# Optimization experiments

Measured on AMD Instinct MI355X. Metric: run time of the kernel, lower is better.

## Reference

```python
import jax, jax.numpy as jnp
import numpy as np

S, C, HD = 2048, 3072, 128
H = C // HD  # 24 heads
EPS = 1e-6


def setup_inputs() -> dict:
    key = jax.random.key(0)
    ks = jax.random.split(key, 12)
    x = jax.random.normal(ks[0], (S, C), dtype=jnp.float32)
    rope = jax.random.normal(ks[1], (S, 1, HD // 2, 2, 2), dtype=jnp.float32)
    w = 0.02
    return {
        "x": x,
        "rope": rope,
        "wq": jax.random.normal(ks[2], (C, C), dtype=jnp.float32) * w,
        "bq": jnp.zeros((C,), dtype=jnp.float32),
        "wk": jax.random.normal(ks[3], (C, C), dtype=jnp.float32) * w,
        "bk": jnp.zeros((C,), dtype=jnp.float32),
        "wv": jax.random.normal(ks[4], (C, C), dtype=jnp.float32) * w,
        "bv": jnp.zeros((C,), dtype=jnp.float32),
        "wo": jax.random.normal(ks[5], (C, C), dtype=jnp.float32) * w,
        "bo": jnp.zeros((C,), dtype=jnp.float32),
        "qn_w": jnp.ones((HD,), dtype=jnp.float32),
        "kn_w": jnp.ones((HD,), dtype=jnp.float32),
    }


def _rmsnorm(t, w):
    # t: [S, H, HD]; normalize over last dim
    ms = jnp.mean(t * t, axis=-1, keepdims=True)
    return t * jax.lax.rsqrt(ms + EPS) * w


def _apply_rotary(t, rope):
    # t: [S, H, HD] -> [S, H, HD//2, 1, 2]; rope: [S, 1, HD//2, 2, 2]
    t_ = t.reshape(S, H, HD // 2, 1, 2)
    out = jnp.sum(rope * t_, axis=-1)  # [S, H, HD//2, 2]
    return out.reshape(S, H, HD)


def reference(x, rope, wq, bq, wk, bk, wv, bv, wo, bo, qn_w, kn_w):
    q = (x @ wq.T + bq).reshape(S, H, HD)
    k = (x @ wk.T + bk).reshape(S, H, HD)
    v = (x @ wv.T + bv).reshape(S, H, HD)
    q = _rmsnorm(q, qn_w)
    k = _rmsnorm(k, kn_w)
    q = _apply_rotary(q, rope)
    k = _apply_rotary(k, rope)
    # dense SDPA: scores [H, S, S]
    scores = jnp.einsum('shd,thd->hst', q, k) / jnp.sqrt(jnp.float32(HD))
    attn = jax.nn.softmax(scores, axis=-1)
    out = jnp.einsum('hst,thd->shd', attn, v).reshape(S, C)
    return out @ wo.T + bo
```

## Files before the change

kernel.cpp:

```cpp
#include <hip/hip_runtime.h>
#include <cstdint>
#include <cstddef>

#define SS 2048
#define CC 3072
#define HDIM 128
#define NH 24

using bf16 = __bf16;
typedef __bf16 bf16x8 __attribute__((ext_vector_type(8)));
typedef float f32x4 __attribute__((ext_vector_type(4)));

typedef const __attribute__((address_space(1))) void* gas1_cvp;
typedef __attribute__((address_space(3))) void* las3_vp;

__device__ __forceinline__ void gll16(const void* g, void* l) {
  __builtin_amdgcn_global_load_lds((gas1_cvp)g, (las3_vp)l, 16, 0, 0);
}

__device__ __forceinline__ bf16x8 cvt8(f32x4 a, f32x4 b) {
  bf16x8 r;
  r[0] = (bf16)a[0]; r[1] = (bf16)a[1]; r[2] = (bf16)a[2]; r[3] = (bf16)a[3];
  r[4] = (bf16)b[0]; r[5] = (bf16)b[1]; r[6] = (bf16)b[2]; r[7] = (bf16)b[3];
  return r;
}

#define NX ((size_t)SS * CC)
#define NW ((size_t)CC * CC)

__global__ __launch_bounds__(256)
void k_cvt(const float* __restrict__ s0, const float* __restrict__ s1,
           const float* __restrict__ s2, const float* __restrict__ s3,
           const float* __restrict__ s4, bf16* __restrict__ dst) {
  const int z = blockIdx.y;
  const float* src = (z == 0) ? s0 : (z == 1) ? s1 : (z == 2) ? s2 : (z == 3) ? s3 : s4;
  const size_t nz = (z == 0) ? NX : NW;
  const size_t base = (z == 0) ? 0 : NX + (size_t)(z - 1) * NW;
  const size_t i = ((size_t)blockIdx.x * 256 + threadIdx.x) * 8;
  if (i < nz) {
    const f32x4 a = *(const f32x4*)(src + i);
    const f32x4 b = *(const f32x4*)(src + i + 4);
    *(bf16x8*)(dst + base + i) = cvt8(a, b);
  }
}

__device__ __forceinline__ void gemm_bt_bf16(const bf16* __restrict__ A,
                                             const bf16* __restrict__ W,
                                             const float* __restrict__ bias,
                                             void* __restrict__ out,
                                             int M, int N, int K, int mode) {
  __shared__ __align__(16) bf16 As[128][32];
  __shared__ __align__(16) bf16 Ws[128][32];
  const int t = threadIdx.x, wave = t >> 6, lane = t & 63;
  const int m0 = blockIdx.y * 128, n0 = blockIdx.x * 128;
  const int wm = (wave >> 1) * 64, wn = (wave & 1) * 64;
  const int fr = lane & 15, fq = (lane >> 4) * 8;

  f32x4 acc[4][4] = {};

  for (int k0 = 0; k0 < K; k0 += 32) {
    __syncthreads();
#pragma unroll
    for (int it = 0; it < 2; ++it) {
      const int pc = wave * 2 + it;
      const int pi = pc * 64 + lane;
      const int row = pi >> 2, c8 = (pi & 3) * 8;
      gll16(A + (size_t)(m0 + row) * K + (k0 + c8), (char*)&As[0][0] + pc * 1024);
      gll16(W + (size_t)(n0 + row) * K + (k0 + c8), (char*)&Ws[0][0] + pc * 1024);
    }
    __syncthreads();
    bf16x8 a[4], b[4];
#pragma unroll
    for (int i = 0; i < 4; ++i) a[i] = *(const bf16x8*)&As[wm + i * 16 + fr][fq];
#pragma unroll
    for (int j = 0; j < 4; ++j) b[j] = *(const bf16x8*)&Ws[wn + j * 16 + fr][fq];
#pragma unroll
    for (int i = 0; i < 4; ++i)
#pragma unroll
      for (int j = 0; j < 4; ++j)
        acc[i][j] = __builtin_amdgcn_mfma_f32_16x16x32_bf16(a[i], b[j], acc[i][j], 0, 0, 0);
  }

  const int lr4 = (lane >> 4) * 4;
#pragma unroll
  for (int i = 0; i < 4; ++i) {
#pragma unroll
    for (int j = 0; j < 4; ++j) {
      const int col = n0 + wn + j * 16 + fr;
      const float bb = bias[col];
#pragma unroll
      for (int r = 0; r < 4; ++r) {
        const int row = m0 + wm + i * 16 + lr4 + r;
        const float v = acc[i][j][r] + bb;
        if (mode == 0)
          ((bf16*)out)[((size_t)(col >> 7) * M + row) * 128 + (col & 127)] = (bf16)v;
        else if (mode == 1)
          ((bf16*)out)[(size_t)col * M + row] = (bf16)v;
        else
          ((float*)out)[(size_t)row * N + col] = v;
      }
    }
  }
}

__global__ __launch_bounds__(256, 2)
void k_gemm_qkv_b(const bf16* __restrict__ xb,
                  const bf16* __restrict__ wqb, const bf16* __restrict__ wkb,
                  const bf16* __restrict__ wvb,
                  const float* __restrict__ bq, const float* __restrict__ bk,
                  const float* __restrict__ bv,
                  bf16* __restrict__ Qo, bf16* __restrict__ Ko, bf16* __restrict__ Vo) {
  const int z = blockIdx.z;
  const bf16* W  = (z == 0) ? wqb : (z == 1) ? wkb : wvb;
  const float* B = (z == 0) ? bq : (z == 1) ? bk : bv;
  void* O        = (z == 0) ? (void*)Qo : (z == 1) ? (void*)Ko : (void*)Vo;
  gemm_bt_bf16(xb, W, B, O, SS, CC, CC, (z == 2) ? 1 : 0);
}

__global__ __launch_bounds__(256, 2)
void k_gemm_out_b(const bf16* __restrict__ A, const bf16* __restrict__ wob,
                  const float* __restrict__ bo, float* __restrict__ out) {
  gemm_bt_bf16(A, wob, bo, out, SS, CC, CC, 2);
}

template<int AF32>
__device__ __forceinline__ void gemm_core(const void* __restrict__ Ap,
                                          const float* __restrict__ W,
                                          const float* __restrict__ bias,
                                          void* __restrict__ out,
                                          int M, int N, int K, int mode) {
  __shared__ __align__(16) bf16 As[128][32];
  __shared__ __align__(16) bf16 Ws[128][32];
  const int t = threadIdx.x, wave = t >> 6, lane = t & 63;
  const int m0 = blockIdx.y * 128, n0 = blockIdx.x * 128;
  const int wm = (wave >> 1) * 64, wn = (wave & 1) * 64;
  const int fr = lane & 15, fq = (lane >> 4) * 8;
  const int pi0 = wave * 128 + lane;
  const int pi1 = pi0 + 64;
  const int row0 = pi0 >> 2, c0 = (pi0 & 3) * 8;
  const int row1 = pi1 >> 2, c1 = (pi1 & 3) * 8;

  f32x4 raf0[2], raf1[2], rw0[2], rw1[2];
  bf16x8 rab0, rab1;

  auto issue = [&](int k0) {
    if (AF32) {
      const float* A = (const float*)Ap;
      const float* p0 = A + (size_t)(m0 + row0) * K + k0 + c0;
      raf0[0] = *(const f32x4*)p0; raf0[1] = *(const f32x4*)(p0 + 4);
      const float* p1 = A + (size_t)(m0 + row1) * K + k0 + c1;
      raf1[0] = *(const f32x4*)p1; raf1[1] = *(const f32x4*)(p1 + 4);
    } else {
      const bf16* A = (const bf16*)Ap;
      rab0 = *(const bf16x8*)(A + (size_t)(m0 + row0) * K + k0 + c0);
      rab1 = *(const bf16x8*)(A + (size_t)(m0 + row1) * K + k0 + c1);
    }
    const float* q0 = W + (size_t)(n0 + row0) * K + k0 + c0;
    rw0[0] = *(const f32x4*)q0; rw0[1] = *(const f32x4*)(q0 + 4);
    const float* q1 = W + (size_t)(n0 + row1) * K + k0 + c1;
    rw1[0] = *(const f32x4*)q1; rw1[1] = *(const f32x4*)(q1 + 4);
  };

  f32x4 acc[4][4] = {};
  issue(0);
  for (int k0 = 0; k0 < K; k0 += 32) {
    __syncthreads();
    if (AF32) {
      *(bf16x8*)&As[row0][c0] = cvt8(raf0[0], raf0[1]);
      *(bf16x8*)&As[row1][c1] = cvt8(raf1[0], raf1[1]);
    } else {
      *(bf16x8*)&As[row0][c0] = rab0;
      *(bf16x8*)&As[row1][c1] = rab1;
    }
    *(bf16x8*)&Ws[row0][c0] = cvt8(rw0[0], rw0[1]);
    *(bf16x8*)&Ws[row1][c1] = cvt8(rw1[0], rw1[1]);
    __syncthreads();
    if (k0 + 32 < K) issue(k0 + 32);
    bf16x8 a[4], b[4];
#pragma unroll
    for (int i = 0; i < 4; ++i) a[i] = *(const bf16x8*)&As[wm + i * 16 + fr][fq];
#pragma unroll
    for (int j = 0; j < 4; ++j) b[j] = *(const bf16x8*)&Ws[wn + j * 16 + fr][fq];
#pragma unroll
    for (int i = 0; i < 4; ++i)
#pragma unroll
      for (int j = 0; j < 4; ++j)
        acc[i][j] = __builtin_amdgcn_mfma_f32_16x16x32_bf16(a[i], b[j], acc[i][j], 0, 0, 0);
  }

  const int lr4 = (lane >> 4) * 4;
#pragma unroll
  for (int i = 0; i < 4; ++i) {
#pragma unroll
    for (int j = 0; j < 4; ++j) {
      const int col = n0 + wn + j * 16 + fr;
      const float bb = bias[col];
#pragma unroll
      for (int r = 0; r < 4; ++r) {
        const int row = m0 + wm + i * 16 + lr4 + r;
        const float v = acc[i][j][r] + bb;
        if (mode == 0)
          ((bf16*)out)[((size_t)(col >> 7) * M + row) * 128 + (col & 127)] = (bf16)v;
        else if (mode == 1)
          ((bf16*)out)[(size_t)col * M + row] = (bf16)v;
        else
          ((float*)out)[(size_t)row * N + col] = v;
      }
    }
  }
}

__global__ __launch_bounds__(256, 2)
void k_gemm_qkv_f(const float* __restrict__ x,
                  const float* __restrict__ wq, const float* __restrict__ wk,
                  const float* __restrict__ wv,
                  const float* __restrict__ bq, const float* __restrict__ bk,
                  const float* __restrict__ bv,
                  bf16* __restrict__ Qo, bf16* __restrict__ Ko, bf16* __restrict__ Vo) {
  const int z = blockIdx.z;
  const float* W = (z == 0) ? wq : (z == 1) ? wk : wv;
  const float* B = (z == 0) ? bq : (z == 1) ? bk : bv;
  void* O        = (z == 0) ? (void*)Qo : (z == 1) ? (void*)Ko : (void*)Vo;
  gemm_core<1>(x, W, B, O, SS, CC, CC, (z == 2) ? 1 : 0);
}

__global__ __launch_bounds__(256, 2)
void k_gemm_out_f(const bf16* __restrict__ A, const float* __restrict__ wo,
                  const float* __restrict__ bo, float* __restrict__ out) {
  gemm_core<0>(A, wo, bo, out, SS, CC, CC, 2);
}

__global__ __launch_bounds__(256)
void k_norm_rope(bf16* __restrict__ Q, bf16* __restrict__ K,
                 const float* __restrict__ rope,
                 const float* __restrict__ qw, const float* __restrict__ kw) {
  const int t = threadIdx.x, wave = t >> 6, lane = t & 63;
  const int idx = blockIdx.x * 4 + wave;
  const int s = idx / NH, h = idx % NH;
  const size_t base = ((size_t)h * SS + s) * HDIM + 2 * lane;

  bf16 q2[2], k2[2];
  *(uint32_t*)q2 = *(const uint32_t*)(Q + base);
  *(uint32_t*)k2 = *(const uint32_t*)(K + base);
  const float q0 = (float)q2[0], q1 = (float)q2[1];
  const float k0 = (float)k2[0], k1 = (float)k2[1];
  float sq = q0 * q0 + q1 * q1;
  float sk = k0 * k0 + k1 * k1;
#pragma unroll
  for (int m = 1; m < 64; m <<= 1) {
    sq += __shfl_xor(sq, m);
    sk += __shfl_xor(sk, m);
  }
  const float rq = rsqrtf(sq * (1.0f / 128.0f) + 1e-6f);
  const float rk = rsqrtf(sk * (1.0f / 128.0f) + 1e-6f);

  const float qn0 = q0 * rq * qw[2 * lane], qn1 = q1 * rq * qw[2 * lane + 1];
  const float kn0 = k0 * rk * kw[2 * lane], kn1 = k1 * rk * kw[2 * lane + 1];

  const f32x4 rp = *(const f32x4*)(rope + (size_t)s * 256 + 4 * lane);
  const float r00 = rp[0], r01 = rp[1], r10 = rp[2], r11 = rp[3];

  const float SC = 0.08838834764831845f * 1.44269504088896340f;
  const float oq0 = (r00 * qn0 + r01 * qn1) * SC;
  const float oq1 = (r10 * qn0 + r11 * qn1) * SC;
  const float ok0 = r00 * kn0 + r01 * kn1;
  const float ok1 = r10 * kn0 + r11 * kn1;

  bf16 wq2[2] = {(bf16)oq0, (bf16)oq1};
  bf16 wk2[2] = {(bf16)ok0, (bf16)ok1};
  *(uint32_t*)(Q + base) = *(uint32_t*)wq2;
  *(uint32_t*)(K + base) = *(uint32_t*)wk2;
}

__global__ __launch_bounds__(256, 2)
void k_attn(const bf16* __restrict__ Q, const bf16* __restrict__ Kt,
            const bf16* __restrict__ Vt, bf16* __restrict__ Out) {
  __shared__ __align__(16) bf16 Ks[4][64][32];
  __shared__ __align__(16) bf16 Vs[2][128][32];
  __shared__ __align__(16) bf16 Ps[64][72];
  const int t = threadIdx.x, wave = t >> 6, lane = t & 63;
  const int h = blockIdx.y, q0 = blockIdx.x * 64;
  const int fr = lane & 15, fq = (lane >> 4) * 8;
  const int lr4 = (lane >> 4) * 4;
  const float FM = 32.0f;

  bf16x8 aq[4];
#pragma unroll
  for (int kc = 0; kc < 4; ++kc)
    aq[kc] = *(const bf16x8*)(Q + ((size_t)h * SS + q0 + wave * 16 + fr) * HDIM + kc * 32 + fq);

  f32x4 oacc[8] = {};
  float lacc[4] = {0.f, 0.f, 0.f, 0.f};

  for (int k0 = 0; k0 < SS; k0 += 64) {
    __syncthreads();
#pragma unroll
    for (int it = 0; it < 4; ++it) {
      const int pc = wave * 4 + it;
      {
        const int row = (pc & 3) * 16 + (lane >> 2);
        const int d8 = (lane & 3) * 8;
        gll16(Kt + ((size_t)h * SS + k0 + row) * HDIM + (pc >> 2) * 32 + d8,
              (char*)&Ks[0][0][0] + pc * 1024);
      }
      {
        const int d = (pc & 7) * 16 + (lane >> 2);
        const int k8 = (lane & 3) * 8;
        gll16(Vt + ((size_t)h * HDIM + d) * SS + k0 + (pc >> 3) * 32 + k8,
              (char*)&Vs[0][0][0] + pc * 1024);
      }
    }
    __syncthreads();

    f32x4 sacc[4] = {};
#pragma unroll
    for (int kc = 0; kc < 4; ++kc) {
#pragma unroll
      for (int jt = 0; jt < 4; ++jt) {
        const bf16x8 b = *(const bf16x8*)&Ks[kc][jt * 16 + fr][fq];
        sacc[jt] = __builtin_amdgcn_mfma_f32_16x16x32_bf16(aq[kc], b, sacc[jt], 0, 0, 0);
      }
    }

#pragma unroll
    for (int r = 0; r < 4; ++r) {
      float ps = 0.f;
#pragma unroll
      for (int jt = 0; jt < 4; ++jt) {
        const float pv = exp2f(sacc[jt][r] - FM);
        sacc[jt][r] = pv;
        ps += pv;
        Ps[wave * 16 + lr4 + r][jt * 16 + fr] = (bf16)pv;
      }
      lacc[r] += ps;
    }
    asm volatile("s_waitcnt lgkmcnt(0)" ::: "memory");

#pragma unroll
    for (int kc = 0; kc < 2; ++kc) {
      const bf16x8 ap = *(const bf16x8*)&Ps[wave * 16 + fr][kc * 32 + fq];
#pragma unroll
      for (int jd = 0; jd < 8; ++jd) {
        const bf16x8 b = *(const bf16x8*)&Vs[kc][jd * 16 + fr][fq];
        oacc[jd] = __builtin_amdgcn_mfma_f32_16x16x32_bf16(ap, b, oacc[jd], 0, 0, 0);
      }
    }
  }

#pragma unroll
  for (int r = 0; r < 4; ++r) {
    float l = lacc[r];
    l += __shfl_xor(l, 1);
    l += __shfl_xor(l, 2);
    l += __shfl_xor(l, 4);
    l += __shfl_xor(l, 8);
    const float inv = 1.0f / l;
    const int row = q0 + wave * 16 + lr4 + r;
#pragma unroll
    for (int jd = 0; jd < 8; ++jd) {
      const int col = h * HDIM + jd * 16 + fr;
      Out[(size_t)row * CC + col] = (bf16)(oacc[jd][r] * inv);
    }
  }
}

extern "C" void kernel_launch(void* const* d_in, const int* in_sizes, int n_in,
                              void* d_out, int out_size, void* d_ws, size_t ws_size,
                              hipStream_t stream) {
  const float* x    = (const float*)d_in[0];
  const float* rope = (const float*)d_in[1];
  const float* wq   = (const float*)d_in[2];
  const float* bq   = (const float*)d_in[3];
  const float* wk   = (const float*)d_in[4];
  const float* bk   = (const float*)d_in[5];
  const float* wv   = (const float*)d_in[6];
  const float* bv   = (const float*)d_in[7];
  const float* wo   = (const float*)d_in[8];
  const float* bo   = (const float*)d_in[9];
  const float* qw   = (const float*)d_in[10];
  const float* kw   = (const float*)d_in[11];

  const size_t need = (4 * NX + 4 * NW) * sizeof(bf16);
  bf16* Vt = (bf16*)d_out;

  if (ws_size >= need) {
    bf16* xb  = (bf16*)d_ws;
    bf16* wqb = xb + NX;
    bf16* wkb = wqb + NW;
    bf16* wvb = wkb + NW;
    bf16* wob = wvb + NW;
    bf16* Qn  = wob + NW;
    bf16* Kn  = Qn + NX;
    bf16* Ao  = Kn + NX;

    k_cvt<<<dim3((unsigned)(NW / 2048), 5), 256, 0, stream>>>(x, wq, wk, wv, wo, xb);
    k_gemm_qkv_b<<<dim3(CC / 128, SS / 128, 3), 256, 0, stream>>>(
        xb, wqb, wkb, wvb, bq, bk, bv, Qn, Kn, Vt);
    k_norm_rope<<<dim3(SS * NH / 4), 256, 0, stream>>>(Qn, Kn, rope, qw, kw);
    k_attn<<<dim3(SS / 64, NH), 256, 0, stream>>>(Qn, Kn, Vt, Ao);
    k_gemm_out_b<<<dim3(CC / 128, SS / 128), 256, 0, stream>>>(Ao, wob, bo, (float*)d_out);
  } else {
    bf16* Qn = (bf16*)d_ws;
    bf16* Kn = Qn + NX;
    bf16* Ao = Kn + NX;

    k_gemm_qkv_f<<<dim3(CC / 128, SS / 128, 3), 256, 0, stream>>>(
        x, wq, wk, wv, bq, bk, bv, Qn, Kn, Vt);
    k_norm_rope<<<dim3(SS * NH / 4), 256, 0, stream>>>(Qn, Kn, rope, qw, kw);
    k_attn<<<dim3(SS / 64, NH), 256, 0, stream>>>(Qn, Kn, Vt, Ao);
    k_gemm_out_f<<<dim3(CC / 128, SS / 128), 256, 0, stream>>>(Ao, wo, bo, (float*)d_out);
  }
}
```

Measured before the change: 556.3 us.

## Deepen GEMM K-tile to 64, raise occupancy bounds, remap attention blocks per XCD

The bf16 GEMM now loads a 64-wide K slab per iteration as two 32-wide LDS planes, halving the barrier count per K. Launch bounds for the GEMMs go to 4 blocks per CU and for attention to 3. Attention moves to a 1D grid where block id modulo 8 picks a group of three heads, so blocks sharing K/V land on the same XCD's L2. A dead store of the exp values back into sacc is removed. The larger LDS tiles and tighter register budgets may cause spills or cap real occupancy.

```diff
diff --git a/kernel.cpp b/kernel.cpp
--- a/kernel.cpp
+++ b/kernel.cpp
@@ -49,8 +49,8 @@
                                              const float* __restrict__ bias,
                                              void* __restrict__ out,
                                              int M, int N, int K, int mode) {
-  __shared__ __align__(16) bf16 As[128][32];
-  __shared__ __align__(16) bf16 Ws[128][32];
+  __shared__ __align__(16) bf16 As[2][128][32];
+  __shared__ __align__(16) bf16 Ws[2][128][32];
   const int t = threadIdx.x, wave = t >> 6, lane = t & 63;
   const int m0 = blockIdx.y * 128, n0 = blockIdx.x * 128;
   const int wm = (wave >> 1) * 64, wn = (wave & 1) * 64;
@@ -58,27 +58,33 @@
 
   f32x4 acc[4][4] = {};
 
-  for (int k0 = 0; k0 < K; k0 += 32) {
-    __syncthreads();
-#pragma unroll
-    for (int it = 0; it < 2; ++it) {
-      const int pc = wave * 2 + it;
-      const int pi = pc * 64 + lane;
-      const int row = pi >> 2, c8 = (pi & 3) * 8;
-      gll16(A + (size_t)(m0 + row) * K + (k0 + c8), (char*)&As[0][0] + pc * 1024);
-      gll16(W + (size_t)(n0 + row) * K + (k0 + c8), (char*)&Ws[0][0] + pc * 1024);
-    }
-    __syncthreads();
-    bf16x8 a[4], b[4];
-#pragma unroll
-    for (int i = 0; i < 4; ++i) a[i] = *(const bf16x8*)&As[wm + i * 16 + fr][fq];
-#pragma unroll
-    for (int j = 0; j < 4; ++j) b[j] = *(const bf16x8*)&Ws[wn + j * 16 + fr][fq];
-#pragma unroll
-    for (int i = 0; i < 4; ++i)
-#pragma unroll
-      for (int j = 0; j < 4; ++j)
-        acc[i][j] = __builtin_amdgcn_mfma_f32_16x16x32_bf16(a[i], b[j], acc[i][j], 0, 0, 0);
+  for (int k0 = 0; k0 < K; k0 += 64) {
+    __syncthreads();
+#pragma unroll
+    for (int it = 0; it < 4; ++it) {
+      const int pc = wave * 4 + it;
+      const int pl = pc >> 3, rb = pc & 7;
+      const int row = rb * 16 + (lane >> 2);
+      const int c8 = (lane & 3) * 8;
+      gll16(A + (size_t)(m0 + row) * K + k0 + pl * 32 + c8,
+            (char*)&As[0][0][0] + pc * 1024);
+      gll16(W + (size_t)(n0 + row) * K + k0 + pl * 32 + c8,
+            (char*)&Ws[0][0][0] + pc * 1024);
+    }
+    __syncthreads();
+#pragma unroll
+    for (int c = 0; c < 2; ++c) {
+      bf16x8 a[4], b[4];
+#pragma unroll
+      for (int i = 0; i < 4; ++i) a[i] = *(const bf16x8*)&As[c][wm + i * 16 + fr][fq];
+#pragma unroll
+      for (int j = 0; j < 4; ++j) b[j] = *(const bf16x8*)&Ws[c][wn + j * 16 + fr][fq];
+#pragma unroll
+      for (int i = 0; i < 4; ++i)
+#pragma unroll
+        for (int j = 0; j < 4; ++j)
+          acc[i][j] = __builtin_amdgcn_mfma_f32_16x16x32_bf16(a[i], b[j], acc[i][j], 0, 0, 0);
+    }
   }
 
   const int lr4 = (lane >> 4) * 4;
@@ -103,7 +109,7 @@
   }
 }
 
-__global__ __launch_bounds__(256, 2)
+__global__ __launch_bounds__(256, 4)
 void k_gemm_qkv_b(const bf16* __restrict__ xb,
                   const bf16* __restrict__ wqb, const bf16* __restrict__ wkb,
                   const bf16* __restrict__ wvb,
@@ -117,7 +123,7 @@
   gemm_bt_bf16(xb, W, B, O, SS, CC, CC, (z == 2) ? 1 : 0);
 }
 
-__global__ __launch_bounds__(256, 2)
+__global__ __launch_bounds__(256, 4)
 void k_gemm_out_b(const bf16* __restrict__ A, const bf16* __restrict__ wob,
                   const float* __restrict__ bo, float* __restrict__ out) {
   gemm_bt_bf16(A, wob, bo, out, SS, CC, CC, 2);
@@ -272,14 +278,17 @@
   *(uint32_t*)(K + base) = *(uint32_t*)wk2;
 }
 
-__global__ __launch_bounds__(256, 2)
+__global__ __launch_bounds__(256, 3)
 void k_attn(const bf16* __restrict__ Q, const bf16* __restrict__ Kt,
             const bf16* __restrict__ Vt, bf16* __restrict__ Out) {
   __shared__ __align__(16) bf16 Ks[4][64][32];
   __shared__ __align__(16) bf16 Vs[2][128][32];
   __shared__ __align__(16) bf16 Ps[64][72];
   const int t = threadIdx.x, wave = t >> 6, lane = t & 63;
-  const int h = blockIdx.y, q0 = blockIdx.x * 64;
+  const int bx = blockIdx.x;
+  const int xg = bx & 7, slot = bx >> 3;
+  const int h = xg * 3 + (slot >> 5);
+  const int q0 = (slot & 31) * 64;
   const int fr = lane & 15, fq = (lane >> 4) * 8;
   const int lr4 = (lane >> 4) * 4;
   const float FM = 32.0f;
@@ -328,7 +337,6 @@
 #pragma unroll
       for (int jt = 0; jt < 4; ++jt) {
         const float pv = exp2f(sacc[jt][r] - FM);
-        sacc[jt][r] = pv;
         ps += pv;
         Ps[wave * 16 + lr4 + r][jt * 16 + fr] = (bf16)pv;
       }
@@ -397,7 +405,7 @@
     k_gemm_qkv_b<<<dim3(CC / 128, SS / 128, 3), 256, 0, stream>>>(
         xb, wqb, wkb, wvb, bq, bk, bv, Qn, Kn, Vt);
     k_norm_rope<<<dim3(SS * NH / 4), 256, 0, stream>>>(Qn, Kn, rope, qw, kw);
-    k_attn<<<dim3(SS / 64, NH), 256, 0, stream>>>(Qn, Kn, Vt, Ao);
+    k_attn<<<dim3((SS / 64) * NH), 256, 0, stream>>>(Qn, Kn, Vt, Ao);
     k_gemm_out_b<<<dim3(CC / 128, SS / 128), 256, 0, stream>>>(Ao, wob, bo, (float*)d_out);
   } else {
     bf16* Qn = (bf16*)d_ws;
@@ -407,7 +415,7 @@
     k_gemm_qkv_f<<<dim3(CC / 128, SS / 128, 3), 256, 0, stream>>>(
         x, wq, wk, wv, bq, bk, bv, Qn, Kn, Vt);
     k_norm_rope<<<dim3(SS * NH / 4), 256, 0, stream>>>(Qn, Kn, rope, qw, kw);
-    k_attn<<<dim3(SS / 64, NH), 256, 0, stream>>>(Qn, Kn, Vt, Ao);
+    k_attn<<<dim3((SS / 64) * NH), 256, 0, stream>>>(Qn, Kn, Vt, Ao);
     k_gemm_out_f<<<dim3(CC / 128, SS / 128), 256, 0, stream>>>(Ao, wo, bo, (float*)d_out);
   }
 }
```

New measurement: 517.5 us. -7.0%, faster.
